# Optimization experiments

Measured on AMD Instinct MI355X. Metric: run time of the kernel, lower is better.

The kernel has to match this reference:

```python
import jax, jax.numpy as jnp
import numpy as np

HIDDEN = 64
N_CODES = 512
COMMIT = 0.25


def _conv(x, w, b, pad):
    y = jax.lax.conv_general_dilated(
        x, w, window_strides=(1, 1), padding=[(pad, pad), (pad, pad)],
        dimension_numbers=('NCHW', 'OIHW', 'NCHW'))
    return y + b[None, :, None, None]


def _vq(z, codebook):
    # z: [B,C,H,W], codebook: [K,C]
    B, C, H, W = z.shape
    z_flat = z.transpose(0, 2, 3, 1).reshape(-1, C)  # [N,C]
    dists = (z_flat ** 2).sum(1, keepdims=True) \
        + (codebook ** 2).sum(1) - 2.0 * z_flat @ codebook.T  # [N,K]
    indices = jnp.argmin(dists, axis=1)
    z_q = codebook[indices].reshape(B, H, W, C).transpose(0, 3, 1, 2)
    commit_loss = jnp.mean((jax.lax.stop_gradient(z_q) - z) ** 2)
    codebook_loss = jnp.mean((z_q - jax.lax.stop_gradient(z)) ** 2)
    vq_loss = codebook_loss + COMMIT * commit_loss
    z_q_st = z + jax.lax.stop_gradient(z_q - z)  # straight-through
    return z_q_st, vq_loss


def setup_inputs() -> dict:
    key = jax.random.key(0)
    ks = jax.random.split(key, 12)
    B, H, W = 16, 128, 128
    s = 0.05
    inp = {
        'x': jax.random.normal(ks[0], (B, 1, H, W), jnp.float32),
        'stem_w': jax.random.normal(ks[1], (HIDDEN, 1, 3, 3), jnp.float32) * s,
        'stem_b': jnp.zeros((HIDDEN,), jnp.float32),
        'up1_w': jax.random.normal(ks[2], (HIDDEN, HIDDEN, 3, 3), jnp.float32) * s,
        'up1_b': jnp.zeros((HIDDEN,), jnp.float32),
        'up2_w': jax.random.normal(ks[3], (HIDDEN, HIDDEN, 1, 1), jnp.float32) * s,
        'up2_b': jnp.zeros((HIDDEN,), jnp.float32),
        'tau_w': jax.random.normal(ks[4], (HIDDEN, HIDDEN, 1, 1), jnp.float32) * s,
        'tau_b': jnp.zeros((HIDDEN,), jnp.float32),
        'codebook': jax.random.uniform(ks[5], (N_CODES, HIDDEN), jnp.float32,
                                       minval=-1.0 / N_CODES, maxval=1.0 / N_CODES),
        'dec_w': jax.random.normal(ks[6], (1, HIDDEN, 1, 1), jnp.float32) * s,
        'dec_b': jnp.zeros((1,), jnp.float32),
        'n_steps': 5,
    }
    return inp


def reference(x, stem_w, stem_b, up1_w, up1_b, up2_w, up2_b,
              tau_w, tau_b, codebook, dec_w, dec_b, n_steps):
    state = jax.nn.relu(_conv(x, stem_w, stem_b, pad=1))
    vq_total = jnp.float32(0.0)
    for _ in range(n_steps):  # 'fixed' mode: exactly n_steps iterations
        delta = _conv(jax.nn.relu(_conv(state, up1_w, up1_b, pad=1)), up2_w, up2_b, pad=0)
        beta = jax.nn.sigmoid(_conv(state, tau_w, tau_b, pad=0))  # tau_scale = 1.0
        state = beta * state + (1.0 - beta) * delta
        state, vq_loss = _vq(state, codebook)
        vq_total = vq_total + vq_loss
    output = jax.nn.sigmoid(_conv(state, dec_w, dec_b, pad=0))
    return output, vq_total / n_steps
```

## Files before the change

kernel.cpp:

```cpp
#include <hip/hip_runtime.h>
#include <hip/hip_bf16.h>
#include <math.h>

typedef unsigned short ushort_t;
typedef __attribute__((ext_vector_type(8))) short short8;
typedef __attribute__((ext_vector_type(4))) float f32x4;
typedef __attribute__((ext_vector_type(4))) int int4v;
#define MFMA __builtin_amdgcn_mfma_f32_16x16x32_bf16

#define NPOS 262144
#define NSTEPS 5

#define OB_S0   4096u
#define OB_S1   (OB_S0 + 33554432u)
#define OB_STG  (OB_S1 + 33554432u)
#define STG_W2  73728u
#define STG_WT  81920u
#define STG_CB  90112u
#define STG_NH  155648u
#define STG_SZ  157696u
#define OB_SWT  (OB_STG + STG_SZ)
#define OB_SBP  (OB_SWT + 2304u)
#define OB_PART (OB_SBP + 256u)
#define DYN_LDS 157760u

static __device__ __forceinline__ int permP(int p) {
  return (p & 0x23) | ((p >> 1) & 0x0c) | ((p & 0x4) << 2);
}
static __device__ __forceinline__ ushort_t f2bf(float f) {
  __hip_bfloat16 h = __float2bfloat16(f);
  return *reinterpret_cast<ushort_t*>(&h);
}
static __device__ __forceinline__ float bf2f(ushort_t h) {
  return __uint_as_float(((unsigned)h) << 16);
}

__global__ void prep_kernel(const float* __restrict__ up1_w, const float* __restrict__ up2_w,
                            const float* __restrict__ tau_w, const float* __restrict__ cb,
                            const float* __restrict__ stem_w, const float* __restrict__ stem_b,
                            char* __restrict__ ws) {
  int id = blockIdx.x * 256 + threadIdx.x;
  ushort_t* stg = (ushort_t*)(ws + OB_STG);
  if (id < 36864) {
    int j = id & 7, lane = (id >> 3) & 63, f = (id >> 9) & 3, s = (id >> 11) & 1, tap = id >> 12;
    int col = lane & 15, kg = lane >> 4;
    stg[id] = f2bf(up1_w[((16 * f + col) * 64 + permP(32 * s + 8 * kg + j)) * 9 + tap]);
  } else if (id < 40960) {
    int jj = id - 36864;
    int j = jj & 7, lane = (jj >> 3) & 63, f = (jj >> 9) & 3, s = (jj >> 11) & 1;
    int col = lane & 15, kg = lane >> 4;
    stg[id] = f2bf(up2_w[(16 * f + col) * 64 + permP(32 * s + 8 * kg + j)]);
  } else if (id < 45056) {
    int jj = id - 40960;
    int j = jj & 7, lane = (jj >> 3) & 63, f = (jj >> 9) & 3, s = (jj >> 11) & 1;
    int col = lane & 15, kg = lane >> 4;
    stg[id] = f2bf(tau_w[(16 * f + col) * 64 + permP(32 * s + 8 * kg + j)]);
  } else if (id < 77824) {
    int jj = id - 45056;
    int j = jj & 7, lane = (jj >> 3) & 63, s = (jj >> 9) & 1, cf = jj >> 10;
    int col = lane & 15, kg = lane >> 4;
    stg[id] = f2bf(cb[(16 * cf + col) * 64 + permP(32 * s + 8 * kg + j)]);
  } else if (id < 78336) {
    int k = id - 77824;
    float s = 0.f;
    for (int c = 0; c < 64; ++c) { float v = cb[k * 64 + c]; s += v * v; }
    ((float*)(ws + OB_STG + STG_NH))[k] = -0.5f * s;
  } else if (id < 78912) {
    int jj = id - 78336; int tap = jj >> 6, slot = jj & 63;
    ((float*)(ws + OB_SWT))[jj] = stem_w[permP(slot) * 9 + tap];
  } else if (id < 78976) {
    int slot = id - 78912;
    ((float*)(ws + OB_SBP))[slot] = stem_b[permP(slot)];
  }
}

__global__ __launch_bounds__(256) void stem_kernel(const float* __restrict__ x,
      const char* __restrict__ wsro, ushort_t* __restrict__ state) {
  const float* swt = (const float*)(wsro + OB_SWT);
  const float* sbp = (const float*)(wsro + OB_SBP);
  int pos = blockIdx.x * 256 + threadIdx.x;
  int b = pos >> 14, hw = pos & 16383, h = hw >> 7, w = hw & 127;
  const float* xb = x + b * 16384;
  float xv[9];
  #pragma unroll
  for (int ky = 0; ky < 3; ++ky) {
    #pragma unroll
    for (int kx = 0; kx < 3; ++kx) {
      int hh = h + ky - 1, ww = w + kx - 1;
      bool ok = (hh >= 0) && (hh < 128) && (ww >= 0) && (ww < 128);
      xv[ky * 3 + kx] = ok ? xb[hh * 128 + ww] : 0.f;
    }
  }
  float acc[64];
  #pragma unroll
  for (int i = 0; i < 64; ++i) acc[i] = sbp[i];
  #pragma unroll
  for (int tap = 0; tap < 9; ++tap) {
    float xt = xv[tap];
    #pragma unroll
    for (int g = 0; g < 16; ++g) {
      f32x4 w4 = *(const f32x4*)(swt + tap * 64 + g * 4);
      #pragma unroll
      for (int j = 0; j < 4; ++j) acc[g * 4 + j] += xt * w4[j];
    }
  }
  ushort_t* op = state + (size_t)pos * 64;
  #pragma unroll
  for (int sg = 0; sg < 8; ++sg) {
    short8 o;
    #pragma unroll
    for (int j = 0; j < 8; ++j) o[j] = (short)f2bf(fmaxf(acc[sg * 8 + j], 0.f));
    *(short8*)(op + sg * 8) = o;
  }
}

__global__ __launch_bounds__(512, 2) void step_kernel(const ushort_t* __restrict__ sin,
      ushort_t* __restrict__ sout, const char* __restrict__ wsro,
      const float* __restrict__ up1_b, const float* __restrict__ up2_b,
      const float* __restrict__ tau_b, float* __restrict__ partials) {
  extern __shared__ char smem[];
  int t = threadIdx.x, lane = t & 63, wv = t >> 6;
  int col = lane & 15, kg = lane >> 4;
  float* red = (float*)(smem + STG_SZ);

  const char* src = wsro + OB_STG;
  for (int it = 0; it < 20; ++it) {
    int c = it * 512 + t;
    if (c < 9856) *(int4v*)(smem + c * 16) = *(const int4v*)(src + c * 16);
  }
  __syncthreads();

  for (int wi = 0; wi < 2; ++wi) {
    int wu = blockIdx.x + wi * 256;
    int lb = ((wu & 7) << 6) + (wu >> 3);
    int b = lb >> 5;
    int row = (lb & 31) * 4 + (wv >> 1);
    int wseg = (wv & 1) * 64;
    const ushort_t* imgbase = sin + (size_t)b * 1048576u;

    f32x4 acc1[4][4] = {};
    #pragma unroll
    for (int ky = 0; ky < 3; ++ky) {
      int h2 = row + ky - 1;
      if (h2 < 0 || h2 > 127) continue;
      const ushort_t* rptr = imgbase + h2 * 8192;
      #pragma unroll
      for (int kx = 0; kx < 3; ++kx) {
        short8 sbf[4][2];
        #pragma unroll
        for (int pf = 0; pf < 4; ++pf) {
          int wloc = wseg + 16 * pf + col + kx - 1;
          const ushort_t* pp = rptr + wloc * 64 + 8 * kg;
          sbf[pf][0] = *(const short8*)(pp);
          sbf[pf][1] = *(const short8*)(pp + 32);
          if ((kx == 0 && pf == 0) || (kx == 2 && pf == 3)) {
            if ((unsigned)wloc >= 128u) {
              short8 z8 = {};
              sbf[pf][0] = z8; sbf[pf][1] = z8;
            }
          }
        }
        int tap = ky * 3 + kx;
        #pragma unroll
        for (int s = 0; s < 2; ++s) {
          #pragma unroll
          for (int f = 0; f < 4; ++f) {
            short8 a = *(const short8*)(smem + ((tap * 2 + s) * 4 + f) * 1024 + lane * 16);
            #pragma unroll
            for (int pf = 0; pf < 4; ++pf)
              acc1[pf][f] = MFMA(a, sbf[pf][s], acc1[pf][f], 0, 0, 0);
          }
        }
      }
    }

    f32x4 b1v[4];
    #pragma unroll
    for (int f = 0; f < 4; ++f) b1v[f] = *(const f32x4*)(up1_b + 16 * f + 4 * kg);
    short8 hb[4][2];
    #pragma unroll
    for (int pf = 0; pf < 4; ++pf) {
      #pragma unroll
      for (int s = 0; s < 2; ++s) {
        short8 v;
        #pragma unroll
        for (int u = 0; u < 2; ++u) {
          int f = 2 * s + u;
          #pragma unroll
          for (int r = 0; r < 4; ++r)
            v[4 * u + r] = (short)f2bf(fmaxf(acc1[pf][f][r] + b1v[f][r], 0.f));
        }
        hb[pf][s] = v;
      }
    }

    short8 zb[4][2];
    #pragma unroll
    for (int pf = 0; pf < 4; ++pf) {
      int wloc = wseg + 16 * pf + col;
      const ushort_t* cp = imgbase + row * 8192 + wloc * 64 + 8 * kg;
      short8 c0 = *(const short8*)(cp);
      short8 c1 = *(const short8*)(cp + 32);
      f32x4 d2[4] = {}, dt[4] = {};
      #pragma unroll
      for (int s = 0; s < 2; ++s) {
        short8 cs = s ? c1 : c0;
        #pragma unroll
        for (int f = 0; f < 4; ++f) {
          short8 wa2 = *(const short8*)(smem + STG_W2 + (s * 4 + f) * 1024 + lane * 16);
          short8 wat = *(const short8*)(smem + STG_WT + (s * 4 + f) * 1024 + lane * 16);
          d2[f] = MFMA(wa2, hb[pf][s], d2[f], 0, 0, 0);
          dt[f] = MFMA(wat, cs, dt[f], 0, 0, 0);
        }
      }
      #pragma unroll
      for (int s = 0; s < 2; ++s) {
        short8 cs = s ? c1 : c0;
        short8 zv;
        #pragma unroll
        for (int u = 0; u < 2; ++u) {
          int f = 2 * s + u;
          f32x4 b2 = *(const f32x4*)(up2_b + 16 * f + 4 * kg);
          f32x4 bt = *(const f32x4*)(tau_b + 16 * f + 4 * kg);
          #pragma unroll
          for (int r = 0; r < 4; ++r) {
            float sv = bf2f((ushort_t)cs[4 * u + r]);
            float xg = dt[f][r] + bt[r];
            float beta = __builtin_amdgcn_rcpf(1.f + __expf(-xg));
            float z = beta * sv + (1.f - beta) * (d2[f][r] + b2[r]);
            zv[4 * u + r] = (short)f2bf(z);
          }
        }
        zb[pf][s] = zv;
      }
    }

    float bd[4] = {-3.0e38f, -3.0e38f, -3.0e38f, -3.0e38f};
    int bki[4] = {0, 0, 0, 0};
    #pragma unroll 2
    for (int cf = 0; cf < 32; ++cf) {
      short8 a0 = *(const short8*)(smem + STG_CB + (cf * 2 + 0) * 1024 + lane * 16);
      short8 a1 = *(const short8*)(smem + STG_CB + (cf * 2 + 1) * 1024 + lane * 16);
      f32x4 cinit = *(const f32x4*)(smem + STG_NH + (16 * cf + 4 * kg) * 4);
      #pragma unroll
      for (int pf = 0; pf < 4; ++pf) {
        f32x4 acc = cinit;
        acc = MFMA(a0, zb[pf][0], acc, 0, 0, 0);
        acc = MFMA(a1, zb[pf][1], acc, 0, 0, 0);
        #pragma unroll
        for (int r = 0; r < 4; ++r) {
          int code = 16 * cf + 4 * kg + r;
          if (acc[r] > bd[pf]) { bd[pf] = acc[r]; bki[pf] = code; }
        }
      }
    }

    float ls = 0.f;
    ushort_t* outbase = sout + (size_t)b * 1048576u + row * 8192;
    #pragma unroll
    for (int pf = 0; pf < 4; ++pf) {
      float d = bd[pf]; int k = bki[pf];
      #pragma unroll
      for (int off = 16; off <= 32; off <<= 1) {
        float od = __shfl_xor(d, off);
        int   ok = __shfl_xor(k, off);
        if (od > d || (od == d && ok < k)) { d = od; k = ok; }
      }
      int cbase = STG_CB + ((k >> 4) * 2) * 1024 + (16 * kg + (k & 15)) * 16;
      short8 q0 = *(const short8*)(smem + cbase);
      short8 q1 = *(const short8*)(smem + cbase + 1024);
      ushort_t* op = outbase + (wseg + 16 * pf + col) * 64 + 8 * kg;
      *(short8*)(op) = q0;
      *(short8*)(op + 32) = q1;
      #pragma unroll
      for (int s = 0; s < 2; ++s) {
        short8 q = s ? q1 : q0;
        short8 zv = zb[pf][s];
        #pragma unroll
        for (int j = 0; j < 8; ++j) {
          float dd = bf2f((ushort_t)q[j]) - bf2f((ushort_t)zv[j]);
          ls += dd * dd;
        }
      }
    }
    #pragma unroll
    for (int off = 1; off < 64; off <<= 1) ls += __shfl_xor(ls, off);
    if (lane == 0) red[wv] = ls;
    __syncthreads();
    if (t == 0) {
      float s = 0.f;
      #pragma unroll
      for (int i = 0; i < 8; ++i) s += red[i];
      partials[wu] = s;
    }
    __syncthreads();
  }
}

__global__ __launch_bounds__(256) void dec_kernel(const ushort_t* __restrict__ state,
      const float* __restrict__ dec_w, const float* __restrict__ dec_b,
      const float* __restrict__ part, float* __restrict__ out) {
  __shared__ float wsm[64];
  __shared__ float rs[256];
  int t = threadIdx.x;
  if (t < 64) wsm[t] = dec_w[permP(t)];
  __syncthreads();
  int wv = t >> 6, lane = t & 63;
  int pl = lane >> 3, sc = lane & 7;
  float b0 = dec_b[0];
  int base0 = blockIdx.x * 256;
  #pragma unroll
  for (int it = 0; it < 8; ++it) {
    int pos = base0 + it * 32 + wv * 8 + pl;
    short8 v = *(const short8*)(state + (size_t)pos * 64 + sc * 8);
    float d = 0.f;
    #pragma unroll
    for (int j = 0; j < 8; ++j) d += bf2f((ushort_t)v[j]) * wsm[sc * 8 + j];
    d += __shfl_xor(d, 1); d += __shfl_xor(d, 2); d += __shfl_xor(d, 4);
    if (sc == 0) out[pos] = __builtin_amdgcn_rcpf(1.f + __expf(-(d + b0)));
  }
  if (blockIdx.x == 0) {
    float v = 0.f;
    for (int i = t; i < 2560; i += 256) v += part[i];
    rs[t] = v;
    __syncthreads();
    for (int w = 128; w >= 1; w >>= 1) {
      if (t < w) rs[t] += rs[t + w];
      __syncthreads();
    }
    if (t == 0) out[NPOS] = rs[0] * 1.25f / (16777216.f * 5.f);
  }
}

extern "C" void kernel_launch(void* const* d_in, const int* in_sizes, int n_in,
                              void* d_out, int out_size, void* d_ws, size_t ws_size,
                              hipStream_t stream) {
  (void)in_sizes; (void)n_in; (void)out_size; (void)ws_size;
  const float* x      = (const float*)d_in[0];
  const float* stem_w = (const float*)d_in[1];
  const float* stem_b = (const float*)d_in[2];
  const float* up1_w  = (const float*)d_in[3];
  const float* up1_b  = (const float*)d_in[4];
  const float* up2_w  = (const float*)d_in[5];
  const float* up2_b  = (const float*)d_in[6];
  const float* tau_w  = (const float*)d_in[7];
  const float* tau_b  = (const float*)d_in[8];
  const float* cb     = (const float*)d_in[9];
  const float* dec_w  = (const float*)d_in[10];
  const float* dec_b  = (const float*)d_in[11];
  float* out = (float*)d_out;
  char*  ws  = (char*)d_ws;

  ushort_t* s0   = (ushort_t*)(ws + OB_S0);
  ushort_t* s1   = (ushort_t*)(ws + OB_S1);
  float*    part = (float*)(ws + OB_PART);

  (void)hipFuncSetAttribute((const void*)step_kernel,
                            hipFuncAttributeMaxDynamicSharedMemorySize, DYN_LDS);

  prep_kernel<<<309, 256, 0, stream>>>(up1_w, up2_w, tau_w, cb, stem_w, stem_b, ws);
  stem_kernel<<<1024, 256, 0, stream>>>(x, ws, s0);
  for (int s = 0; s < NSTEPS; ++s) {
    const ushort_t* in  = (s & 1) ? s1 : s0;
    ushort_t*       o   = (s & 1) ? s0 : s1;
    step_kernel<<<256, 512, DYN_LDS, stream>>>(in, o, ws, up1_b, up2_b, tau_b,
                                               part + s * 512);
  }
  dec_kernel<<<1024, 256, 0, stream>>>(s1, dec_w, dec_b, part, out);
}
```

Baseline: 394.9 us.

## Shrink step kernel LDS footprint and launch one block per work unit

The step kernel now stages only the codebook and the up2 weights in shared memory. The 3x3 conv weights, tau weights and codebook norms are read directly from global memory. LDS use drops from about 154KB to about 72KB, so two 512-thread blocks can share a CU. The grid doubles to 512 blocks, each handling one work unit instead of looping over two. The aim is to raise occupancy and let loads overlap across blocks, at the cost of more global/L2 traffic for the weight reads inside the conv inner loop.

```diff
diff --git a/kernel.cpp b/kernel.cpp
--- a/kernel.cpp
+++ b/kernel.cpp
@@ -22,7 +22,9 @@
 #define OB_SWT  (OB_STG + STG_SZ)
 #define OB_SBP  (OB_SWT + 2304u)
 #define OB_PART (OB_SBP + 256u)
-#define DYN_LDS 157760u
+#define LDS_W2  65536u
+#define LDS_RED 73728u
+#define DYN_LDS 73760u
 
 static __device__ __forceinline__ int permP(int p) {
   return (p & 0x23) | ((p >> 1) & 0x0c) | ((p & 0x4) << 2);
@@ -121,179 +123,182 @@
   extern __shared__ char smem[];
   int t = threadIdx.x, lane = t & 63, wv = t >> 6;
   int col = lane & 15, kg = lane >> 4;
-  float* red = (float*)(smem + STG_SZ);
-
-  const char* src = wsro + OB_STG;
-  for (int it = 0; it < 20; ++it) {
+  float* red = (float*)(smem + LDS_RED);
+
+  const char* srcCB = wsro + OB_STG + STG_CB;
+  #pragma unroll
+  for (int it = 0; it < 8; ++it) {
     int c = it * 512 + t;
-    if (c < 9856) *(int4v*)(smem + c * 16) = *(const int4v*)(src + c * 16);
-  }
+    *(int4v*)(smem + c * 16) = *(const int4v*)(srcCB + c * 16);
+  }
+  *(int4v*)(smem + LDS_W2 + t * 16) = *(const int4v*)(wsro + OB_STG + STG_W2 + t * 16);
   __syncthreads();
 
-  for (int wi = 0; wi < 2; ++wi) {
-    int wu = blockIdx.x + wi * 256;
-    int lb = ((wu & 7) << 6) + (wu >> 3);
-    int b = lb >> 5;
-    int row = (lb & 31) * 4 + (wv >> 1);
-    int wseg = (wv & 1) * 64;
-    const ushort_t* imgbase = sin + (size_t)b * 1048576u;
-
-    f32x4 acc1[4][4] = {};
-    #pragma unroll
-    for (int ky = 0; ky < 3; ++ky) {
-      int h2 = row + ky - 1;
-      if (h2 < 0 || h2 > 127) continue;
-      const ushort_t* rptr = imgbase + h2 * 8192;
-      #pragma unroll
-      for (int kx = 0; kx < 3; ++kx) {
-        short8 sbf[4][2];
-        #pragma unroll
-        for (int pf = 0; pf < 4; ++pf) {
-          int wloc = wseg + 16 * pf + col + kx - 1;
-          const ushort_t* pp = rptr + wloc * 64 + 8 * kg;
-          sbf[pf][0] = *(const short8*)(pp);
-          sbf[pf][1] = *(const short8*)(pp + 32);
-          if ((kx == 0 && pf == 0) || (kx == 2 && pf == 3)) {
-            if ((unsigned)wloc >= 128u) {
-              short8 z8 = {};
-              sbf[pf][0] = z8; sbf[pf][1] = z8;
-            }
+  const ushort_t* w1g = (const ushort_t*)(wsro + OB_STG);
+  const ushort_t* wtg = (const ushort_t*)(wsro + OB_STG + STG_WT);
+  const float*    nhg = (const float*)(wsro + OB_STG + STG_NH);
+
+  int wu = blockIdx.x;
+  int lb = ((wu & 7) << 6) | (wu >> 3);
+  int b = lb >> 5;
+  int row = (lb & 31) * 4 + (wv >> 1);
+  int wseg = (wv & 1) * 64;
+  const ushort_t* imgbase = sin + (size_t)b * 1048576u;
+
+  f32x4 acc1[4][4] = {};
+  #pragma unroll
+  for (int ky = 0; ky < 3; ++ky) {
+    int h2 = row + ky - 1;
+    if (h2 < 0 || h2 > 127) continue;
+    const ushort_t* rptr = imgbase + h2 * 8192;
+    #pragma unroll
+    for (int kx = 0; kx < 3; ++kx) {
+      short8 sbf[4][2];
+      #pragma unroll
+      for (int pf = 0; pf < 4; ++pf) {
+        int wloc = wseg + 16 * pf + col + kx - 1;
+        const ushort_t* pp = rptr + wloc * 64 + 8 * kg;
+        sbf[pf][0] = *(const short8*)(pp);
+        sbf[pf][1] = *(const short8*)(pp + 32);
+        if ((kx == 0 && pf == 0) || (kx == 2 && pf == 3)) {
+          if ((unsigned)wloc >= 128u) {
+            short8 z8 = {};
+            sbf[pf][0] = z8; sbf[pf][1] = z8;
           }
         }
-        int tap = ky * 3 + kx;
-        #pragma unroll
-        for (int s = 0; s < 2; ++s) {
-          #pragma unroll
-          for (int f = 0; f < 4; ++f) {
-            short8 a = *(const short8*)(smem + ((tap * 2 + s) * 4 + f) * 1024 + lane * 16);
-            #pragma unroll
-            for (int pf = 0; pf < 4; ++pf)
-              acc1[pf][f] = MFMA(a, sbf[pf][s], acc1[pf][f], 0, 0, 0);
-          }
-        }
-      }
-    }
-
-    f32x4 b1v[4];
-    #pragma unroll
-    for (int f = 0; f < 4; ++f) b1v[f] = *(const f32x4*)(up1_b + 16 * f + 4 * kg);
-    short8 hb[4][2];
-    #pragma unroll
-    for (int pf = 0; pf < 4; ++pf) {
+      }
+      int tap = ky * 3 + kx;
       #pragma unroll
       for (int s = 0; s < 2; ++s) {
-        short8 v;
-        #pragma unroll
-        for (int u = 0; u < 2; ++u) {
-          int f = 2 * s + u;
-          #pragma unroll
-          for (int r = 0; r < 4; ++r)
-            v[4 * u + r] = (short)f2bf(fmaxf(acc1[pf][f][r] + b1v[f][r], 0.f));
-        }
-        hb[pf][s] = v;
-      }
-    }
-
-    short8 zb[4][2];
-    #pragma unroll
-    for (int pf = 0; pf < 4; ++pf) {
-      int wloc = wseg + 16 * pf + col;
-      const ushort_t* cp = imgbase + row * 8192 + wloc * 64 + 8 * kg;
-      short8 c0 = *(const short8*)(cp);
-      short8 c1 = *(const short8*)(cp + 32);
-      f32x4 d2[4] = {}, dt[4] = {};
-      #pragma unroll
-      for (int s = 0; s < 2; ++s) {
-        short8 cs = s ? c1 : c0;
         #pragma unroll
         for (int f = 0; f < 4; ++f) {
-          short8 wa2 = *(const short8*)(smem + STG_W2 + (s * 4 + f) * 1024 + lane * 16);
-          short8 wat = *(const short8*)(smem + STG_WT + (s * 4 + f) * 1024 + lane * 16);
-          d2[f] = MFMA(wa2, hb[pf][s], d2[f], 0, 0, 0);
-          dt[f] = MFMA(wat, cs, dt[f], 0, 0, 0);
+          short8 a = *(const short8*)(w1g + ((tap * 2 + s) * 4 + f) * 512 + lane * 8);
+          #pragma unroll
+          for (int pf = 0; pf < 4; ++pf)
+            acc1[pf][f] = MFMA(a, sbf[pf][s], acc1[pf][f], 0, 0, 0);
         }
       }
-      #pragma unroll
-      for (int s = 0; s < 2; ++s) {
-        short8 cs = s ? c1 : c0;
-        short8 zv;
+    }
+  }
+
+  f32x4 b1v[4];
+  #pragma unroll
+  for (int f = 0; f < 4; ++f) b1v[f] = *(const f32x4*)(up1_b + 16 * f + 4 * kg);
+  short8 hb[4][2];
+  #pragma unroll
+  for (int pf = 0; pf < 4; ++pf) {
+    #pragma unroll
+    for (int s = 0; s < 2; ++s) {
+      short8 v;
+      #pragma unroll
+      for (int u = 0; u < 2; ++u) {
+        int f = 2 * s + u;
         #pragma unroll
-        for (int u = 0; u < 2; ++u) {
-          int f = 2 * s + u;
-          f32x4 b2 = *(const f32x4*)(up2_b + 16 * f + 4 * kg);
-          f32x4 bt = *(const f32x4*)(tau_b + 16 * f + 4 * kg);
-          #pragma unroll
-          for (int r = 0; r < 4; ++r) {
-            float sv = bf2f((ushort_t)cs[4 * u + r]);
-            float xg = dt[f][r] + bt[r];
-            float beta = __builtin_amdgcn_rcpf(1.f + __expf(-xg));
-            float z = beta * sv + (1.f - beta) * (d2[f][r] + b2[r]);
-            zv[4 * u + r] = (short)f2bf(z);
-          }
-        }
-        zb[pf][s] = zv;
-      }
-    }
-
-    float bd[4] = {-3.0e38f, -3.0e38f, -3.0e38f, -3.0e38f};
-    int bki[4] = {0, 0, 0, 0};
-    #pragma unroll 2
-    for (int cf = 0; cf < 32; ++cf) {
-      short8 a0 = *(const short8*)(smem + STG_CB + (cf * 2 + 0) * 1024 + lane * 16);
-      short8 a1 = *(const short8*)(smem + STG_CB + (cf * 2 + 1) * 1024 + lane * 16);
-      f32x4 cinit = *(const f32x4*)(smem + STG_NH + (16 * cf + 4 * kg) * 4);
-      #pragma unroll
-      for (int pf = 0; pf < 4; ++pf) {
-        f32x4 acc = cinit;
-        acc = MFMA(a0, zb[pf][0], acc, 0, 0, 0);
-        acc = MFMA(a1, zb[pf][1], acc, 0, 0, 0);
+        for (int r = 0; r < 4; ++r)
+          v[4 * u + r] = (short)f2bf(fmaxf(acc1[pf][f][r] + b1v[f][r], 0.f));
+      }
+      hb[pf][s] = v;
+    }
+  }
+
+  short8 zb[4][2];
+  #pragma unroll
+  for (int pf = 0; pf < 4; ++pf) {
+    int wloc = wseg + 16 * pf + col;
+    const ushort_t* cp = imgbase + row * 8192 + wloc * 64 + 8 * kg;
+    short8 c0 = *(const short8*)(cp);
+    short8 c1 = *(const short8*)(cp + 32);
+    f32x4 d2[4] = {}, dt[4] = {};
+    #pragma unroll
+    for (int s = 0; s < 2; ++s) {
+      short8 cs = s ? c1 : c0;
+      #pragma unroll
+      for (int f = 0; f < 4; ++f) {
+        short8 wa2 = *(const short8*)(smem + LDS_W2 + (s * 4 + f) * 1024 + lane * 16);
+        short8 wat = *(const short8*)(wtg + (s * 4 + f) * 512 + lane * 8);
+        d2[f] = MFMA(wa2, hb[pf][s], d2[f], 0, 0, 0);
+        dt[f] = MFMA(wat, cs, dt[f], 0, 0, 0);
+      }
+    }
+    #pragma unroll
+    for (int s = 0; s < 2; ++s) {
+      short8 cs = s ? c1 : c0;
+      short8 zv;
+      #pragma unroll
+      for (int u = 0; u < 2; ++u) {
+        int f = 2 * s + u;
+        f32x4 b2 = *(const f32x4*)(up2_b + 16 * f + 4 * kg);
+        f32x4 bt = *(const f32x4*)(tau_b + 16 * f + 4 * kg);
         #pragma unroll
         for (int r = 0; r < 4; ++r) {
-          int code = 16 * cf + 4 * kg + r;
-          if (acc[r] > bd[pf]) { bd[pf] = acc[r]; bki[pf] = code; }
+          float sv = bf2f((ushort_t)cs[4 * u + r]);
+          float xg = dt[f][r] + bt[r];
+          float beta = __builtin_amdgcn_rcpf(1.f + __expf(-xg));
+          float z = beta * sv + (1.f - beta) * (d2[f][r] + b2[r]);
+          zv[4 * u + r] = (short)f2bf(z);
         }
       }
-    }
-
-    float ls = 0.f;
-    ushort_t* outbase = sout + (size_t)b * 1048576u + row * 8192;
+      zb[pf][s] = zv;
+    }
+  }
+
+  float bd[4] = {-3.0e38f, -3.0e38f, -3.0e38f, -3.0e38f};
+  int bki[4] = {0, 0, 0, 0};
+  #pragma unroll 2
+  for (int cf = 0; cf < 32; ++cf) {
+    short8 a0 = *(const short8*)(smem + (cf * 2 + 0) * 1024 + lane * 16);
+    short8 a1 = *(const short8*)(smem + (cf * 2 + 1) * 1024 + lane * 16);
+    f32x4 cinit = *(const f32x4*)(nhg + 16 * cf + 4 * kg);
     #pragma unroll
     for (int pf = 0; pf < 4; ++pf) {
-      float d = bd[pf]; int k = bki[pf];
-      #pragma unroll
-      for (int off = 16; off <= 32; off <<= 1) {
-        float od = __shfl_xor(d, off);
-        int   ok = __shfl_xor(k, off);
-        if (od > d || (od == d && ok < k)) { d = od; k = ok; }
-      }
-      int cbase = STG_CB + ((k >> 4) * 2) * 1024 + (16 * kg + (k & 15)) * 16;
-      short8 q0 = *(const short8*)(smem + cbase);
-      short8 q1 = *(const short8*)(smem + cbase + 1024);
-      ushort_t* op = outbase + (wseg + 16 * pf + col) * 64 + 8 * kg;
-      *(short8*)(op) = q0;
-      *(short8*)(op + 32) = q1;
-      #pragma unroll
-      for (int s = 0; s < 2; ++s) {
-        short8 q = s ? q1 : q0;
-        short8 zv = zb[pf][s];
-        #pragma unroll
-        for (int j = 0; j < 8; ++j) {
-          float dd = bf2f((ushort_t)q[j]) - bf2f((ushort_t)zv[j]);
-          ls += dd * dd;
-        }
-      }
-    }
-    #pragma unroll
-    for (int off = 1; off < 64; off <<= 1) ls += __shfl_xor(ls, off);
-    if (lane == 0) red[wv] = ls;
-    __syncthreads();
-    if (t == 0) {
-      float s = 0.f;
-      #pragma unroll
-      for (int i = 0; i < 8; ++i) s += red[i];
-      partials[wu] = s;
-    }
-    __syncthreads();
+      f32x4 acc = cinit;
+      acc = MFMA(a0, zb[pf][0], acc, 0, 0, 0);
+      acc = MFMA(a1, zb[pf][1], acc, 0, 0, 0);
+      #pragma unroll
+      for (int r = 0; r < 4; ++r) {
+        int code = 16 * cf + 4 * kg + r;
+        if (acc[r] > bd[pf]) { bd[pf] = acc[r]; bki[pf] = code; }
+      }
+    }
+  }
+
+  float ls = 0.f;
+  ushort_t* outbase = sout + (size_t)b * 1048576u + row * 8192;
+  #pragma unroll
+  for (int pf = 0; pf < 4; ++pf) {
+    float d = bd[pf]; int k = bki[pf];
+    #pragma unroll
+    for (int off = 16; off <= 32; off <<= 1) {
+      float od = __shfl_xor(d, off);
+      int   ok = __shfl_xor(k, off);
+      if (od > d || (od == d && ok < k)) { d = od; k = ok; }
+    }
+    int cbase = (k >> 4) * 2048 + (16 * kg + (k & 15)) * 16;
+    short8 q0 = *(const short8*)(smem + cbase);
+    short8 q1 = *(const short8*)(smem + cbase + 1024);
+    ushort_t* op = outbase + (wseg + 16 * pf + col) * 64 + 8 * kg;
+    *(short8*)(op) = q0;
+    *(short8*)(op + 32) = q1;
+    #pragma unroll
+    for (int s = 0; s < 2; ++s) {
+      short8 q = s ? q1 : q0;
+      short8 zv = zb[pf][s];
+      #pragma unroll
+      for (int j = 0; j < 8; ++j) {
+        float dd = bf2f((ushort_t)q[j]) - bf2f((ushort_t)zv[j]);
+        ls += dd * dd;
+      }
+    }
+  }
+  #pragma unroll
+  for (int off = 1; off < 64; off <<= 1) ls += __shfl_xor(ls, off);
+  if (lane == 0) red[wv] = ls;
+  __syncthreads();
+  if (t == 0) {
+    float s = 0.f;
+    #pragma unroll
+    for (int i = 0; i < 8; ++i) s += red[i];
+    partials[wu] = s;
   }
 }
 
@@ -363,7 +368,7 @@
   for (int s = 0; s < NSTEPS; ++s) {
     const ushort_t* in  = (s & 1) ? s1 : s0;
     ushort_t*       o   = (s & 1) ? s0 : s1;
-    step_kernel<<<256, 512, DYN_LDS, stream>>>(in, o, ws, up1_b, up2_b, tau_b,
+    step_kernel<<<512, 512, DYN_LDS, stream>>>(in, o, ws, up1_b, up2_b, tau_b,
                                                part + s * 512);
   }
   dec_kernel<<<1024, 256, 0, stream>>>(s1, dec_w, dec_b, part, out);
```

After: 440.8 us. 11.6% more time.
